# Kernel optimization log

Hardware: AMD Instinct MI355X
Metric: run time of the kernel (lower is better)

## Reference

```python
import jax, jax.numpy as jnp
import numpy as np

SEMANTIC_DIM = 128
N_COMPONENTS = 2
EMBED_DIM = SEMANTIC_DIM * N_COMPONENTS  # 256
MAX_LEN = 512


def sinusoidal_pe(max_len, d_model):
    pos = jnp.arange(max_len, dtype=jnp.float32)[:, None]              # (L,1)
    div = jnp.exp(jnp.arange(0, d_model, 2, dtype=jnp.float32) * (-np.log(10000.0) / d_model))
    ang = pos * div                                                     # (L, d/2)
    # interleave sin/cos: pe[:,0::2]=sin, pe[:,1::2]=cos
    return jnp.stack([jnp.sin(ang), jnp.cos(ang)], axis=-1).reshape(max_len, d_model)


def setup_inputs() -> dict:
    key = jax.random.key(0)
    k1, k2, k3, k4 = jax.random.split(key, 4)
    byte_sequence = jax.random.randint(k1, (64, 512), 0, 256, dtype=jnp.int64)
    continuous_positions = jax.random.uniform(k2, (64, 2048), dtype=jnp.float32)
    emb_table = jax.random.normal(k3, (256, EMBED_DIM), dtype=jnp.float32)
    locality_shapes = jax.random.normal(k4, (256, 3), dtype=jnp.float32)
    return {
        "byte_sequence": byte_sequence,
        "continuous_positions": continuous_positions,
        "emb_table": emb_table,
        "locality_shapes": locality_shapes,
    }


def reference(byte_sequence, continuous_positions, emb_table, locality_shapes):
    B, L = byte_sequence.shape
    pe = sinusoidal_pe(MAX_LEN, EMBED_DIM)[:L]                          # (L, E)
    byte_embeds = emb_table[byte_sequence] + pe[None, :, :]             # (B, L, E)
    byte_amplitudes = byte_embeds.reshape(B, L, N_COMPONENTS, SEMANTIC_DIM)

    byte_positions = jnp.linspace(0.0, 1.0, L, dtype=jnp.float32)      # (L,)
    x_diff = continuous_positions[:, :, None] - byte_positions[None, None, :]  # (B, P, L)

    lp = locality_shapes[byte_sequence]                                 # (B, L, 3)
    widths = jnp.abs(lp[:, :, 1]) * 0.02 + 1e-5                         # (B, L)
    amplitudes = jax.nn.sigmoid(lp[:, :, 2])                            # (B, L)

    local_basis = jnp.exp(-0.5 * (x_diff / widths[:, None, :]) ** 2) * amplitudes[:, None, :]
    semantic_field = jnp.einsum('bpl,blcd->bpcd', local_basis, byte_amplitudes)
    return semantic_field
```

## Files before the change

### kernel.cpp

```cpp
#include <hip/hip_runtime.h>
#include <math.h>

#define LSEQ 512
#define EDIM 256
#define PDIM 2048
#define BM   128
#define BK   32
#define NT   16

typedef _Float16 f16x8 __attribute__((ext_vector_type(8)));
typedef _Float16 f16x2 __attribute__((ext_vector_type(2)));
typedef float    f32x4 __attribute__((ext_vector_type(4)));

#if __has_builtin(__builtin_amdgcn_exp2f)
#define EXP2F(x) __builtin_amdgcn_exp2f(x)
#else
#define EXP2F(x) __expf((x) * 0.6931471805599453f)
#endif

__device__ inline f16x2 pk2(float a, float b) {
#if __has_builtin(__builtin_amdgcn_cvt_pkrtz)
    return __builtin_bit_cast(f16x2, __builtin_amdgcn_cvt_pkrtz(a, b));
#else
    f16x2 r; r[0] = (_Float16)a; r[1] = (_Float16)b; return r;
#endif
}

__device__ inline float hw_sin(float ang) {
#if __has_builtin(__builtin_amdgcn_sinf)
    float rev = ang * 0.15915494309189535f;
    return __builtin_amdgcn_sinf(rev - floorf(rev));
#else
    return sinf(ang);
#endif
}
__device__ inline float hw_cos(float ang) {
#if __has_builtin(__builtin_amdgcn_cosf)
    float rev = ang * 0.15915494309189535f;
    return __builtin_amdgcn_cosf(rev - floorf(rev));
#else
    return cosf(ang);
#endif
}

__device__ __host__ inline int tile_off(int r, int g) {
    return ((r >> 1) << 6) + ((r & 1) << 5) + (((g ^ ((r >> 1) & 3)) & 3) << 3);
}

__device__ inline void g2lds16(const void* g, void* l) {
    __builtin_amdgcn_global_load_lds(
        (const __attribute__((address_space(1))) void*)g,
        (__attribute__((address_space(3))) void*)l, 16, 0, 0);
}

__global__ __launch_bounds__(256) void precompute_all(
    const int*   __restrict__ bs,
    const float* __restrict__ ls,
    const float* __restrict__ emb,
    float2*      __restrict__ params,
    _Float16*    __restrict__ baset) {
    const int b   = blockIdx.x >> 4;
    const int t   = blockIdx.x & 15;
    const int tid = threadIdx.x;

    __shared__ int sByte[BK];
    if (tid < BK) {
        const int l    = t * BK + tid;
        const int byte = bs[b * LSEQ + l];
        sByte[tid] = byte;
        const float l1  = ls[byte * 3 + 1];
        const float l2  = ls[byte * 3 + 2];
        const float wdt = fabsf(l1) * 0.02f + 1e-5f;
        const float amp = 1.0f / (1.0f + __expf(-l2));
        params[b * LSEQ + l] = make_float2(-0.72134752f / (wdt * wdt),
                                           __log2f(amp));
    }
    __syncthreads();

    const float div = __expf((float)(tid >> 1) * (-2.0f * 9.210340372f / 256.0f));
    _Float16* chunk = baset + ((size_t)blockIdx.x << 13);
#pragma unroll
    for (int g = 0; g < 4; ++g) {
        f16x8 v;
#pragma unroll
        for (int j = 0; j < 8; ++j) {
            const int lj  = g * 8 + j;
            const float ang = (float)(t * BK + lj) * div;
            const float pev = (tid & 1) ? hw_cos(ang) : hw_sin(ang);
            v[j] = (_Float16)(emb[sByte[lj] * EDIM + tid] + pev);
        }
        *(f16x8*)&chunk[tile_off(tid, g)] = v;
    }
}

__global__ __launch_bounds__(512, 4) void field_mfma(
    const float*    __restrict__ cpos,
    const float2*   __restrict__ params,
    const _Float16* __restrict__ baset,
    float*          __restrict__ out) {

    __shared__ __align__(16) _Float16 sW[2][BM * BK];
    __shared__ __align__(16) _Float16 sB[2][EDIM * BK];

    const int orig = blockIdx.x;
    const int wg   = (orig & 7) * 128 + (orig >> 3);
    const int b    = wg >> 4;
    const int pt   = wg & 15;

    const int tid = threadIdx.x, lane = tid & 63, wave = tid >> 6;
    const int c15 = lane & 15, g4 = lane >> 4;
    const int wrow = wave >> 2, wcol = wave & 3;

    const int sp = tid >> 2;
    const int sg = tid & 3;
    const float mypos = cpos[b * PDIM + pt * BM + sp];
    const float invL  = 1.0f / (float)(LSEQ - 1);
    const int   woff  = tile_off(sp, sg);

    int aoff4[4], boff4[4];
#pragma unroll
    for (int rt = 0; rt < 4; ++rt) aoff4[rt] = tile_off(wrow * 64 + rt * 16 + c15, g4);
#pragma unroll
    for (int ct = 0; ct < 4; ++ct) boff4[ct] = tile_off(wcol * 64 + ct * 16 + c15, g4);

    const float2* prm = params + b * LSEQ;
    const _Float16* bt = baset + ((size_t)b * NT << 13);

#pragma unroll
    for (int buf = 0; buf < 2; ++buf) {
        const _Float16* src = bt + buf * 8192 + wave * 1024 + lane * 8;
        g2lds16(src,       &sB[buf][wave * 1024]);
        g2lds16(src + 512, &sB[buf][wave * 1024 + 512]);
    }

    float4 qn0, qn1, qn2, qn3;
    {
        const float4* qp = (const float4*)(prm + sg * 8);
        qn0 = qp[0]; qn1 = qp[1]; qn2 = qp[2]; qn3 = qp[3];
    }

    auto genW = [&](int t, int dbuf) {
        const float bl0 = (float)(t * BK + sg * 8) * invL;
        const float pd  = mypos - bl0;
        float w[8];
#define GW(i, c2, la) { float d = pd - (float)(i) * invL; \
                        w[i] = EXP2F(fmaf(d * d, (c2), (la))); }
        GW(0, qn0.x, qn0.y) GW(1, qn0.z, qn0.w)
        GW(2, qn1.x, qn1.y) GW(3, qn1.z, qn1.w)
        GW(4, qn2.x, qn2.y) GW(5, qn2.z, qn2.w)
        GW(6, qn3.x, qn3.y) GW(7, qn3.z, qn3.w)
#undef GW
        f16x8 wv;
        ((f16x2*)&wv)[0] = pk2(w[0], w[1]);
        ((f16x2*)&wv)[1] = pk2(w[2], w[3]);
        ((f16x2*)&wv)[2] = pk2(w[4], w[5]);
        ((f16x2*)&wv)[3] = pk2(w[6], w[7]);
        *(f16x8*)&sW[dbuf][woff] = wv;
    };

    genW(0, 0);
    {
        const float4* qp = (const float4*)(prm + BK + sg * 8);
        qn0 = qp[0]; qn1 = qp[1]; qn2 = qp[2]; qn3 = qp[3];
    }
    __syncthreads();

    f32x4 acc[4][4];
#pragma unroll
    for (int i = 0; i < 4; ++i)
#pragma unroll
        for (int j = 0; j < 4; ++j) acc[i][j] = (f32x4)(0.f);

    for (int t = 0; t < NT; ++t) {
        const int cur = t & 1;
        if (t < NT - 1) genW(t + 1, cur ^ 1);

        const _Float16* wb = sW[cur];
        const _Float16* bb = sB[cur];
        f16x8 af[4];
#pragma unroll
        for (int rt = 0; rt < 4; ++rt) af[rt] = *(const f16x8*)&wb[aoff4[rt]];
        __builtin_amdgcn_s_setprio(1);
#pragma unroll
        for (int ct = 0; ct < 4; ++ct) {
            const f16x8 bf = *(const f16x8*)&bb[boff4[ct]];
#pragma unroll
            for (int rt = 0; rt < 4; ++rt)
                acc[rt][ct] = __builtin_amdgcn_mfma_f32_16x16x32_f16(af[rt], bf, acc[rt][ct], 0, 0, 0);
        }
        __builtin_amdgcn_s_setprio(0);

        __syncthreads();

        if (t < NT - 2) {
            const _Float16* src = bt + (t + 2) * 8192 + wave * 1024 + lane * 8;
            g2lds16(src,       &sB[cur][wave * 1024]);
            g2lds16(src + 512, &sB[cur][wave * 1024 + 512]);
            const float4* qp = (const float4*)(prm + (t + 2) * BK + sg * 8);
            qn0 = qp[0]; qn1 = qp[1]; qn2 = qp[2]; qn3 = qp[3];
        }
    }

#pragma unroll
    for (int rt = 0; rt < 4; ++rt)
#pragma unroll
        for (int ct = 0; ct < 4; ++ct) {
            const int e = wcol * 64 + ct * 16 + c15;
#pragma unroll
            for (int reg = 0; reg < 4; ++reg) {
                const int p = pt * BM + wrow * 64 + rt * 16 + g4 * 4 + reg;
                out[((size_t)b * PDIM + p) * EDIM + e] = acc[rt][ct][reg];
            }
        }
}

extern "C" void kernel_launch(void* const* d_in, const int* in_sizes, int n_in,
                              void* d_out, int out_size, void* d_ws, size_t ws_size,
                              hipStream_t stream) {
    const int*   bs   = (const int*)d_in[0];
    const float* cpos = (const float*)d_in[1];
    const float* emb  = (const float*)d_in[2];
    const float* ls   = (const float*)d_in[3];

    const int B = in_sizes[0] / LSEQ;

    char* ws = (char*)d_ws;
    float2*   params = (float2*)ws;
    _Float16* baset  = (_Float16*)(ws + (1u << 18));

    precompute_all<<<B * NT, 256, 0, stream>>>(bs, ls, emb, params, baset);
    field_mfma<<<B * (PDIM / BM), 512, 0, stream>>>(cpos, params, baset, (float*)d_out);
}
```

Before: 72.95 us.

## Split embedding dimension across two blocks and stage params in LDS

Each workgroup now computes half of the 256-wide embedding output, doubling the grid and halving the accumulator registers and the B-tile LDS footprint. The launch-bounds occupancy hint rises to 6 workgroups. Per-byte Gaussian parameters are loaded once into shared memory instead of being prefetched from global into registers each tile. The trade-off is that each block still regenerates the full exp-based weight tile, so the transcendental work is duplicated across the two halves.

After: 63.77 us (median of 2 runs). 12.6% less time.

```diff
diff --git a/kernel.cpp b/kernel.cpp
--- a/kernel.cpp
+++ b/kernel.cpp
@@ -93,19 +93,21 @@
     }
 }
 
-__global__ __launch_bounds__(512, 4) void field_mfma(
+__global__ __launch_bounds__(512, 6) void field_mfma(
     const float*    __restrict__ cpos,
     const float2*   __restrict__ params,
     const _Float16* __restrict__ baset,
     float*          __restrict__ out) {
 
     __shared__ __align__(16) _Float16 sW[2][BM * BK];
-    __shared__ __align__(16) _Float16 sB[2][EDIM * BK];
+    __shared__ __align__(16) _Float16 sB[2][128 * BK];
+    __shared__ __align__(16) float2   sPrm[LSEQ];
 
     const int orig = blockIdx.x;
-    const int wg   = (orig & 7) * 128 + (orig >> 3);
-    const int b    = wg >> 4;
-    const int pt   = wg & 15;
+    const int wg   = (orig & 7) * 256 + (orig >> 3);
+    const int b    = wg >> 5;
+    const int pt   = (wg >> 1) & 15;
+    const int et   = wg & 1;
 
     const int tid = threadIdx.x, lane = tid & 63, wave = tid >> 6;
     const int c15 = lane & 15, g4 = lane >> 4;
@@ -117,38 +119,33 @@
     const float invL  = 1.0f / (float)(LSEQ - 1);
     const int   woff  = tile_off(sp, sg);
 
-    int aoff4[4], boff4[4];
+    int aoff4[4], boff2[2];
 #pragma unroll
     for (int rt = 0; rt < 4; ++rt) aoff4[rt] = tile_off(wrow * 64 + rt * 16 + c15, g4);
 #pragma unroll
-    for (int ct = 0; ct < 4; ++ct) boff4[ct] = tile_off(wcol * 64 + ct * 16 + c15, g4);
-
-    const float2* prm = params + b * LSEQ;
-    const _Float16* bt = baset + ((size_t)b * NT << 13);
-
+    for (int ct = 0; ct < 2; ++ct) boff2[ct] = tile_off(wcol * 32 + ct * 16 + c15, g4);
+
+    sPrm[tid] = params[b * LSEQ + tid];
+    const _Float16* bt = baset + ((size_t)b * NT << 13) + et * 4096;
 #pragma unroll
     for (int buf = 0; buf < 2; ++buf) {
-        const _Float16* src = bt + buf * 8192 + wave * 1024 + lane * 8;
-        g2lds16(src,       &sB[buf][wave * 1024]);
-        g2lds16(src + 512, &sB[buf][wave * 1024 + 512]);
-    }
-
-    float4 qn0, qn1, qn2, qn3;
-    {
-        const float4* qp = (const float4*)(prm + sg * 8);
-        qn0 = qp[0]; qn1 = qp[1]; qn2 = qp[2]; qn3 = qp[3];
-    }
+        const _Float16* src = bt + buf * 8192 + wave * 512 + lane * 8;
+        g2lds16(src, &sB[buf][wave * 512]);
+    }
+    __syncthreads();
 
     auto genW = [&](int t, int dbuf) {
+        const float4* qp = (const float4*)&sPrm[t * BK + sg * 8];
+        const float4 q0 = qp[0], q1 = qp[1], q2 = qp[2], q3 = qp[3];
         const float bl0 = (float)(t * BK + sg * 8) * invL;
         const float pd  = mypos - bl0;
         float w[8];
 #define GW(i, c2, la) { float d = pd - (float)(i) * invL; \
                         w[i] = EXP2F(fmaf(d * d, (c2), (la))); }
-        GW(0, qn0.x, qn0.y) GW(1, qn0.z, qn0.w)
-        GW(2, qn1.x, qn1.y) GW(3, qn1.z, qn1.w)
-        GW(4, qn2.x, qn2.y) GW(5, qn2.z, qn2.w)
-        GW(6, qn3.x, qn3.y) GW(7, qn3.z, qn3.w)
+        GW(0, q0.x, q0.y) GW(1, q0.z, q0.w)
+        GW(2, q1.x, q1.y) GW(3, q1.z, q1.w)
+        GW(4, q2.x, q2.y) GW(5, q2.z, q2.w)
+        GW(6, q3.x, q3.y) GW(7, q3.z, q3.w)
 #undef GW
         f16x8 wv;
         ((f16x2*)&wv)[0] = pk2(w[0], w[1]);
@@ -159,17 +156,13 @@
     };
 
     genW(0, 0);
-    {
-        const float4* qp = (const float4*)(prm + BK + sg * 8);
-        qn0 = qp[0]; qn1 = qp[1]; qn2 = qp[2]; qn3 = qp[3];
-    }
     __syncthreads();
 
-    f32x4 acc[4][4];
+    f32x4 acc[4][2];
 #pragma unroll
     for (int i = 0; i < 4; ++i)
 #pragma unroll
-        for (int j = 0; j < 4; ++j) acc[i][j] = (f32x4)(0.f);
+        for (int j = 0; j < 2; ++j) acc[i][j] = (f32x4)(0.f);
 
     for (int t = 0; t < NT; ++t) {
         const int cur = t & 1;
@@ -182,8 +175,8 @@
         for (int rt = 0; rt < 4; ++rt) af[rt] = *(const f16x8*)&wb[aoff4[rt]];
         __builtin_amdgcn_s_setprio(1);
 #pragma unroll
-        for (int ct = 0; ct < 4; ++ct) {
-            const f16x8 bf = *(const f16x8*)&bb[boff4[ct]];
+        for (int ct = 0; ct < 2; ++ct) {
+            const f16x8 bf = *(const f16x8*)&bb[boff2[ct]];
 #pragma unroll
             for (int rt = 0; rt < 4; ++rt)
                 acc[rt][ct] = __builtin_amdgcn_mfma_f32_16x16x32_f16(af[rt], bf, acc[rt][ct], 0, 0, 0);
@@ -193,19 +186,16 @@
         __syncthreads();
 
         if (t < NT - 2) {
-            const _Float16* src = bt + (t + 2) * 8192 + wave * 1024 + lane * 8;
-            g2lds16(src,       &sB[cur][wave * 1024]);
-            g2lds16(src + 512, &sB[cur][wave * 1024 + 512]);
-            const float4* qp = (const float4*)(prm + (t + 2) * BK + sg * 8);
-            qn0 = qp[0]; qn1 = qp[1]; qn2 = qp[2]; qn3 = qp[3];
+            const _Float16* src = bt + (t + 2) * 8192 + wave * 512 + lane * 8;
+            g2lds16(src, &sB[cur][wave * 512]);
         }
     }
 
 #pragma unroll
     for (int rt = 0; rt < 4; ++rt)
 #pragma unroll
-        for (int ct = 0; ct < 4; ++ct) {
-            const int e = wcol * 64 + ct * 16 + c15;
+        for (int ct = 0; ct < 2; ++ct) {
+            const int e = et * 128 + wcol * 32 + ct * 16 + c15;
 #pragma unroll
             for (int reg = 0; reg < 4; ++reg) {
                 const int p = pt * BM + wrow * 64 + rt * 16 + g4 * 4 + reg;
@@ -229,5 +219,6 @@
     _Float16* baset  = (_Float16*)(ws + (1u << 18));
 
     precompute_all<<<B * NT, 256, 0, stream>>>(bs, ls, emb, params, baset);
-    field_mfma<<<B * (PDIM / BM), 512, 0, stream>>>(cpos, params, baset, (float*)d_out);
-}
+    const int nblocks = B * (PDIM / BM) * 2;
+    field_mfma<<<nblocks, 512, 0, stream>>>(cpos, params, baset, (float*)d_out);
+}
```

## Halve P tile to 64 rows, stage params in LDS, raise occupancy

Applied to the files above, without the earlier changes.

Shrinks the per-block P tile from 128 to 64 positions, which doubles the grid to 2048 blocks and halves the accumulators per wave. It raises the launch-bounds occupancy hint from 4 to 6. Per-byte parameters are now loaded once into shared memory instead of being fetched from global memory every iteration. Each thread generates 4 weights instead of 8, so the embedding tile in LDS is reused across half as many rows and the total B-tile traffic from global memory doubles.

New measurement: 66.10 us. 9.4% less time.

```diff
diff --git a/kernel.cpp b/kernel.cpp
--- a/kernel.cpp
+++ b/kernel.cpp
@@ -4,11 +4,12 @@
 #define LSEQ 512
 #define EDIM 256
 #define PDIM 2048
-#define BM   128
+#define BP   64
 #define BK   32
 #define NT   16
 
 typedef _Float16 f16x8 __attribute__((ext_vector_type(8)));
+typedef _Float16 f16x4 __attribute__((ext_vector_type(4)));
 typedef _Float16 f16x2 __attribute__((ext_vector_type(2)));
 typedef float    f32x4 __attribute__((ext_vector_type(4)));
 
@@ -93,81 +94,70 @@
     }
 }
 
-__global__ __launch_bounds__(512, 4) void field_mfma(
+__global__ __launch_bounds__(512, 6) void field_mfma(
     const float*    __restrict__ cpos,
     const float2*   __restrict__ params,
     const _Float16* __restrict__ baset,
     float*          __restrict__ out) {
 
-    __shared__ __align__(16) _Float16 sW[2][BM * BK];
+    __shared__ __align__(16) _Float16 sW[2][BP * BK];
     __shared__ __align__(16) _Float16 sB[2][EDIM * BK];
+    __shared__ __align__(16) float2   sPrm[LSEQ];
 
     const int orig = blockIdx.x;
-    const int wg   = (orig & 7) * 128 + (orig >> 3);
-    const int b    = wg >> 4;
-    const int pt   = wg & 15;
+    const int wg   = (orig & 7) * 256 + (orig >> 3);
+    const int b    = wg >> 5;
+    const int ptile= wg & 31;
 
     const int tid = threadIdx.x, lane = tid & 63, wave = tid >> 6;
     const int c15 = lane & 15, g4 = lane >> 4;
     const int wrow = wave >> 2, wcol = wave & 3;
 
-    const int sp = tid >> 2;
-    const int sg = tid & 3;
-    const float mypos = cpos[b * PDIM + pt * BM + sp];
+    const int sp = tid >> 3;
+    const int sg = tid & 7;
+    const float mypos = cpos[b * PDIM + ptile * BP + sp];
     const float invL  = 1.0f / (float)(LSEQ - 1);
-    const int   woff  = tile_off(sp, sg);
-
-    int aoff4[4], boff4[4];
-#pragma unroll
-    for (int rt = 0; rt < 4; ++rt) aoff4[rt] = tile_off(wrow * 64 + rt * 16 + c15, g4);
-#pragma unroll
-    for (int ct = 0; ct < 4; ++ct) boff4[ct] = tile_off(wcol * 64 + ct * 16 + c15, g4);
-
-    const float2* prm = params + b * LSEQ;
+    const int   woff  = tile_off(sp, sg >> 1) + (sg & 1) * 4;
+
+    int aoff[2], boff[4];
+#pragma unroll
+    for (int rt = 0; rt < 2; ++rt) aoff[rt] = tile_off(wrow * 32 + rt * 16 + c15, g4);
+#pragma unroll
+    for (int ct = 0; ct < 4; ++ct) boff[ct] = tile_off(wcol * 64 + ct * 16 + c15, g4);
+
+    sPrm[tid] = params[b * LSEQ + tid];
     const _Float16* bt = baset + ((size_t)b * NT << 13);
-
 #pragma unroll
     for (int buf = 0; buf < 2; ++buf) {
         const _Float16* src = bt + buf * 8192 + wave * 1024 + lane * 8;
         g2lds16(src,       &sB[buf][wave * 1024]);
         g2lds16(src + 512, &sB[buf][wave * 1024 + 512]);
     }
-
-    float4 qn0, qn1, qn2, qn3;
-    {
-        const float4* qp = (const float4*)(prm + sg * 8);
-        qn0 = qp[0]; qn1 = qp[1]; qn2 = qp[2]; qn3 = qp[3];
-    }
+    __syncthreads();
 
     auto genW = [&](int t, int dbuf) {
-        const float bl0 = (float)(t * BK + sg * 8) * invL;
+        const float4* qp = (const float4*)&sPrm[t * BK + sg * 4];
+        const float4 q01 = qp[0], q23 = qp[1];
+        const float bl0 = (float)(t * BK + sg * 4) * invL;
         const float pd  = mypos - bl0;
-        float w[8];
+        float w[4];
 #define GW(i, c2, la) { float d = pd - (float)(i) * invL; \
                         w[i] = EXP2F(fmaf(d * d, (c2), (la))); }
-        GW(0, qn0.x, qn0.y) GW(1, qn0.z, qn0.w)
-        GW(2, qn1.x, qn1.y) GW(3, qn1.z, qn1.w)
-        GW(4, qn2.x, qn2.y) GW(5, qn2.z, qn2.w)
-        GW(6, qn3.x, qn3.y) GW(7, qn3.z, qn3.w)
+        GW(0, q01.x, q01.y) GW(1, q01.z, q01.w)
+        GW(2, q23.x, q23.y) GW(3, q23.z, q23.w)
 #undef GW
-        f16x8 wv;
+        f16x4 wv;
         ((f16x2*)&wv)[0] = pk2(w[0], w[1]);
         ((f16x2*)&wv)[1] = pk2(w[2], w[3]);
-        ((f16x2*)&wv)[2] = pk2(w[4], w[5]);
-        ((f16x2*)&wv)[3] = pk2(w[6], w[7]);
-        *(f16x8*)&sW[dbuf][woff] = wv;
+        *(f16x4*)&sW[dbuf][woff] = wv;
     };
 
     genW(0, 0);
-    {
-        const float4* qp = (const float4*)(prm + BK + sg * 8);
-        qn0 = qp[0]; qn1 = qp[1]; qn2 = qp[2]; qn3 = qp[3];
-    }
     __syncthreads();
 
-    f32x4 acc[4][4];
-#pragma unroll
-    for (int i = 0; i < 4; ++i)
+    f32x4 acc[2][4];
+#pragma unroll
+    for (int i = 0; i < 2; ++i)
 #pragma unroll
         for (int j = 0; j < 4; ++j) acc[i][j] = (f32x4)(0.f);
 
@@ -177,15 +167,15 @@
 
         const _Float16* wb = sW[cur];
         const _Float16* bb = sB[cur];
-        f16x8 af[4];
-#pragma unroll
-        for (int rt = 0; rt < 4; ++rt) af[rt] = *(const f16x8*)&wb[aoff4[rt]];
+        f16x8 af[2];
+#pragma unroll
+        for (int rt = 0; rt < 2; ++rt) af[rt] = *(const f16x8*)&wb[aoff[rt]];
         __builtin_amdgcn_s_setprio(1);
 #pragma unroll
         for (int ct = 0; ct < 4; ++ct) {
-            const f16x8 bf = *(const f16x8*)&bb[boff4[ct]];
-#pragma unroll
-            for (int rt = 0; rt < 4; ++rt)
+            const f16x8 bf = *(const f16x8*)&bb[boff[ct]];
+#pragma unroll
+            for (int rt = 0; rt < 2; ++rt)
                 acc[rt][ct] = __builtin_amdgcn_mfma_f32_16x16x32_f16(af[rt], bf, acc[rt][ct], 0, 0, 0);
         }
         __builtin_amdgcn_s_setprio(0);
@@ -196,19 +186,17 @@
             const _Float16* src = bt + (t + 2) * 8192 + wave * 1024 + lane * 8;
             g2lds16(src,       &sB[cur][wave * 1024]);
             g2lds16(src + 512, &sB[cur][wave * 1024 + 512]);
-            const float4* qp = (const float4*)(prm + (t + 2) * BK + sg * 8);
-            qn0 = qp[0]; qn1 = qp[1]; qn2 = qp[2]; qn3 = qp[3];
-        }
-    }
-
-#pragma unroll
-    for (int rt = 0; rt < 4; ++rt)
+        }
+    }
+
+#pragma unroll
+    for (int rt = 0; rt < 2; ++rt)
 #pragma unroll
         for (int ct = 0; ct < 4; ++ct) {
             const int e = wcol * 64 + ct * 16 + c15;
 #pragma unroll
             for (int reg = 0; reg < 4; ++reg) {
-                const int p = pt * BM + wrow * 64 + rt * 16 + g4 * 4 + reg;
+                const int p = ptile * BP + wrow * 32 + rt * 16 + g4 * 4 + reg;
                 out[((size_t)b * PDIM + p) * EDIM + e] = acc[rt][ct][reg];
             }
         }
@@ -229,5 +217,6 @@
     _Float16* baset  = (_Float16*)(ws + (1u << 18));
 
     precompute_all<<<B * NT, 256, 0, stream>>>(bs, ls, emb, params, baset);
-    field_mfma<<<B * (PDIM / BM), 512, 0, stream>>>(cpos, params, baset, (float*)d_out);
-}
+    const int nblocks = B * (PDIM / BP);
+    field_mfma<<<nblocks, 512, 0, stream>>>(cpos, params, baset, (float*)d_out);
+}
```
